# Optimization experiments

Measured on AMD Instinct MI355X. Metric: run time of the kernel, lower is better.

Reference implementation:

```python
import jax, jax.numpy as jnp
import numpy as np

LOW_DIM, SKIP_DIM, OUT_DIM = 512, 256, 256
EPS_IDW = 1e-8
EPS_LN = 1e-5
K = 3


def setup_inputs() -> dict:
    key = jax.random.key(0)
    ks = jax.random.split(key, 10)
    B, N, S = 4, 8192, 2048
    xyz_hi = jax.random.uniform(ks[0], (B, N, 3), dtype=jnp.float32)
    xyz_lo = jax.random.uniform(ks[1], (B, S, 3), dtype=jnp.float32)
    feat_skip = jax.random.normal(ks[2], (B, N, SKIP_DIM), dtype=jnp.float32)
    feat_lo = jax.random.normal(ks[3], (B, S, LOW_DIM), dtype=jnp.float32)
    in_dim = LOW_DIM + SKIP_DIM
    W1 = jax.random.normal(ks[4], (in_dim, OUT_DIM), dtype=jnp.float32) / np.sqrt(in_dim)
    b1 = jnp.zeros((OUT_DIM,), dtype=jnp.float32)
    W2 = jax.random.normal(ks[5], (OUT_DIM, OUT_DIM), dtype=jnp.float32) / np.sqrt(OUT_DIM)
    b2 = jnp.zeros((OUT_DIM,), dtype=jnp.float32)
    gamma = jnp.ones((OUT_DIM,), dtype=jnp.float32)
    beta = jnp.zeros((OUT_DIM,), dtype=jnp.float32)
    return {"xyz_hi": xyz_hi, "xyz_lo": xyz_lo, "feat_skip": feat_skip,
            "feat_lo": feat_lo, "W1": W1, "b1": b1, "W2": W2, "b2": b2,
            "gamma": gamma, "beta": beta}


def _layer_norm(x, gamma, beta):
    mu = jnp.mean(x, axis=-1, keepdims=True)
    var = jnp.mean(jnp.square(x - mu), axis=-1, keepdims=True)
    return (x - mu) * jax.lax.rsqrt(var + EPS_LN) * gamma + beta


def reference(xyz_hi, xyz_lo, feat_skip, feat_lo, W1, b1, W2, b2, gamma, beta):
    B, N, _ = xyz_hi.shape
    _, S, _ = xyz_lo.shape
    if S == 1:
        interpolated = jnp.broadcast_to(feat_lo, (B, N, feat_lo.shape[-1]))
    else:
        # pairwise Euclidean distances: (B, N, S)
        d2 = (jnp.sum(xyz_hi ** 2, -1)[:, :, None]
              + jnp.sum(xyz_lo ** 2, -1)[:, None, :]
              - 2.0 * jnp.einsum('bnd,bsd->bns', xyz_hi, xyz_lo))
        dists = jnp.sqrt(jnp.maximum(d2, 0.0))
        # smallest-3 via top_k on negated distances
        neg_d, knn_idx = jax.lax.top_k(-dists, K)          # (B, N, 3)
        dk = -neg_d
        inv_d = 1.0 / (dk + EPS_IDW)
        weights = inv_d / jnp.sum(inv_d, axis=-1, keepdims=True)  # (B, N, 3)
        # gather neighbor features: (B, N, 3, low_dim)
        knn_feat = feat_lo[jnp.arange(B)[:, None, None], knn_idx]
        interpolated = jnp.einsum('bnk,bnkc->bnc', weights, knn_feat)
    fused = jnp.concatenate([feat_skip, interpolated], axis=-1)   # (B, N, skip+low)
    h = jax.nn.relu(fused @ W1 + b1)
    h = h @ W2 + b2
    return _layer_norm(h, gamma, beta)
```

## Files before the change

kernel.cpp:

```cpp
#include <hip/hip_runtime.h>
#include <hip/hip_bf16.h>
#include <stdint.h>

typedef unsigned short u16;
typedef __attribute__((ext_vector_type(8))) short short8;
typedef __attribute__((ext_vector_type(4))) float f32x4;

#define BB 4
#define NN 8192
#define SS 2048
#define MTOT 32768
#define CSKIP 256
#define CLO 512
#define CIN 768
#define COUT 256

__device__ __forceinline__ u16 f2bf(float f) {
  unsigned u = __float_as_uint(f);
  u += 0x7fffu + ((u >> 16) & 1u);
  return (u16)(u >> 16);
}

__device__ __forceinline__ void gl_lds16(const void* g, void* l) {
  __builtin_amdgcn_global_load_lds(
      (const __attribute__((address_space(1))) void*)g,
      (__attribute__((address_space(3))) void*)l, 16, 0, 0);
}

__global__ __launch_bounds__(256) void wconv_kernel(const float* __restrict__ W1,
                                                    const float* __restrict__ W2,
                                                    u16* __restrict__ W1aT,
                                                    u16* __restrict__ W1bT,
                                                    u16* __restrict__ W2T) {
  int i = blockIdx.x * 256 + threadIdx.x;
  if (i < 65536) {
    int n = i >> 8, k = i & 255;
    W1aT[i] = f2bf(W1[(size_t)k * COUT + n]);
  } else if (i < 65536 + 131072) {
    int j = i - 65536;
    int n = j >> 9, k = j & 511;
    W1bT[j] = f2bf(W1[(size_t)(256 + k) * COUT + n]);
  } else {
    int j = i - 65536 - 131072;
    int n = j >> 8, k = j & 255;
    W2T[j] = f2bf(W2[(size_t)k * COUT + n]);
  }
}

__global__ __launch_bounds__(512) void knn_kernel(
    const float* __restrict__ xyz_hi, const float* __restrict__ xyz_lo,
    float* __restrict__ wq_g, int* __restrict__ iq_g) {
  __shared__ float4 sxyz[SS];
  __shared__ float md[8][64][3];
  __shared__ int   mi[8][64][3];

  int tid = threadIdx.x;
  int blk = blockIdx.x;
  int b = blk >> 7;
  const float* xl = xyz_lo + (size_t)b * SS * 3;
  for (int j = tid; j < SS; j += 512)
    sxyz[j] = make_float4(xl[j * 3 + 0], xl[j * 3 + 1], xl[j * 3 + 2], 0.f);
  __syncthreads();

  int wave = tid >> 6, lane = tid & 63;
  int qm = blk * 64 + lane;
  float qx = xyz_hi[(size_t)qm * 3 + 0];
  float qy = xyz_hi[(size_t)qm * 3 + 1];
  float qz = xyz_hi[(size_t)qm * 3 + 2];

  float b0 = 1e30f, b1 = 1e30f, b2 = 1e30f;
  int i0 = -1, i1 = -1, i2 = -1;
  int j0 = wave * 256;
#pragma unroll 8
  for (int jj = 0; jj < 256; ++jj) {
    int j = j0 + jj;
    float4 p = sxyz[j];
    float dx = p.x - qx, dy = p.y - qy, dz = p.z - qz;
    float d = fmaf(dx, dx, fmaf(dy, dy, dz * dz));
    bool c0 = d < b0, c1 = d < b1, c2 = d < b2;
    float nb0 = fminf(b0, d);
    float nb1 = __builtin_amdgcn_fmed3f(b0, b1, d);
    float nb2 = __builtin_amdgcn_fmed3f(b1, b2, d);
    int ni0 = c0 ? j : i0;
    int ni1 = c0 ? i0 : (c1 ? j : i1);
    int ni2 = c1 ? i1 : (c2 ? j : i2);
    b0 = nb0; b1 = nb1; b2 = nb2;
    i0 = ni0; i1 = ni1; i2 = ni2;
  }
  md[wave][lane][0] = b0; mi[wave][lane][0] = i0;
  md[wave][lane][1] = b1; mi[wave][lane][1] = i1;
  md[wave][lane][2] = b2; mi[wave][lane][2] = i2;
  __syncthreads();

  if (tid < 64) {
    int q = tid;
    float fb0 = 1e30f, fb1 = 1e30f, fb2 = 1e30f;
    int fi0 = -1, fi1 = -1, fi2 = -1;
    for (int p = 0; p < 8; ++p)
#pragma unroll
      for (int s = 0; s < 3; ++s) {
        float d = md[p][q][s]; int ix = mi[p][q][s];
        if (d < fb2 || (d == fb2 && ix < fi2)) {
          fb2 = d; fi2 = ix;
          if (fb2 < fb1 || (fb2 == fb1 && fi2 < fi1)) {
            float t = fb1; fb1 = fb2; fb2 = t; int ti = fi1; fi1 = fi2; fi2 = ti;
          }
          if (fb1 < fb0 || (fb1 == fb0 && fi1 < fi0)) {
            float t = fb0; fb0 = fb1; fb1 = t; int ti = fi0; fi0 = fi1; fi1 = ti;
          }
        }
      }
    int qm2 = blk * 64 + q;
    float d0 = sqrtf(fb0), d1 = sqrtf(fb1), d2 = sqrtf(fb2);
    float inv0 = 1.0f / (d0 + 1e-8f);
    float inv1 = 1.0f / (d1 + 1e-8f);
    float inv2 = 1.0f / (d2 + 1e-8f);
    float s = inv0 + inv1 + inv2;
    wq_g[(size_t)qm2 * 3 + 0] = inv0 / s;
    wq_g[(size_t)qm2 * 3 + 1] = inv1 / s;
    wq_g[(size_t)qm2 * 3 + 2] = inv2 / s;
    iq_g[(size_t)qm2 * 3 + 0] = fi0;
    iq_g[(size_t)qm2 * 3 + 1] = fi1;
    iq_g[(size_t)qm2 * 3 + 2] = fi2;
  }
}

__global__ __launch_bounds__(256, 4) void ggemm_kernel(
    const float* __restrict__ feat_lo, const u16* __restrict__ W1bT,
    float* __restrict__ G) {
  __shared__ u16 As[32 * 40];
  __shared__ u16 Bs[256 * 32];
  int tid = threadIdx.x;
  int m0 = blockIdx.x << 5;
  int w = tid >> 6, lane = tid & 63;
  int quad = lane >> 4, l16 = lane & 15;

  int srow = tid >> 3, s4 = (tid & 7) << 2;
  const float* arow = feat_lo + (size_t)(m0 + srow) * CLO + s4;
  u16* As_dst = As + srow * 40 + s4;

  f32x4 zero = {0.f, 0.f, 0.f, 0.f};
  f32x4 acc[2][4];
#pragma unroll
  for (int tm = 0; tm < 2; ++tm)
#pragma unroll
    for (int tn = 0; tn < 4; ++tn) acc[tm][tn] = zero;

  for (int kc = 0; kc < 16; ++kc) {
    __syncthreads();
#pragma unroll
    for (int r = 0; r < 4; ++r) {
      int u = tid + r * 256;
      int nrow = u >> 2, c = u & 3;
      int cg = c ^ (nrow & 3);
      gl_lds16(W1bT + (size_t)nrow * CLO + kc * 32 + cg * 8, (char*)Bs + u * 16);
    }
    float4 av = *(const float4*)(arow + kc * 32);
    union { __hip_bfloat162 h2[2]; uint2 u2; } pk;
    pk.h2[0] = __float22bfloat162_rn(make_float2(av.x, av.y));
    pk.h2[1] = __float22bfloat162_rn(make_float2(av.z, av.w));
    *(uint2*)As_dst = pk.u2;
    __syncthreads();

    short8 af[2], bf[4];
#pragma unroll
    for (int t = 0; t < 2; ++t)
      af[t] = *(const short8*)(As + (t * 16 + l16) * 40 + quad * 8);
#pragma unroll
    for (int t = 0; t < 4; ++t) {
      int rr = w * 64 + t * 16 + l16;
      bf[t] = *(const short8*)(Bs + (rr * 4 + (quad ^ (rr & 3))) * 8);
    }
#pragma unroll
    for (int tm = 0; tm < 2; ++tm)
#pragma unroll
      for (int tn = 0; tn < 4; ++tn)
        acc[tm][tn] = __builtin_amdgcn_mfma_f32_16x16x32_bf16(af[tm], bf[tn], acc[tm][tn], 0, 0, 0);
  }

#pragma unroll
  for (int tm = 0; tm < 2; ++tm)
#pragma unroll
    for (int tn = 0; tn < 4; ++tn) {
      int col = w * 64 + tn * 16 + l16;
#pragma unroll
      for (int r = 0; r < 4; ++r) {
        int row = m0 + tm * 16 + quad * 4 + r;
        G[(size_t)row * COUT + col] = acc[tm][tn][r];
      }
    }
}

__global__ __launch_bounds__(256, 2) void gemm1p_kernel(
    const float* __restrict__ feat_skip, const u16* __restrict__ W1aT,
    const float* __restrict__ b1, const float* __restrict__ G,
    const float* __restrict__ wq_g, const int* __restrict__ iq_g,
    u16* __restrict__ H) {
  __shared__ u16 As[64 * 40];
  __shared__ u16 Bs[256 * 32];
  __shared__ float swq[192];
  __shared__ int   siq[192];
  int tid = threadIdx.x;
  int m0 = blockIdx.x << 6;
  int bS = (m0 >> 13) * SS;
  int w = tid >> 6, lane = tid & 63;
  int quad = lane >> 4, l16 = lane & 15;

  if (tid < 192) {
    swq[tid] = wq_g[(size_t)m0 * 3 + tid];
    siq[tid] = iq_g[(size_t)m0 * 3 + tid];
  }

  int srow = tid >> 2, sc8 = (tid & 3) << 3;
  const float* arow = feat_skip + (size_t)(m0 + srow) * CSKIP + sc8;
  u16* As_dst = As + srow * 40 + sc8;

  f32x4 zero = {0.f, 0.f, 0.f, 0.f};
  f32x4 acc[4][4];
#pragma unroll
  for (int tm = 0; tm < 4; ++tm)
#pragma unroll
    for (int tn = 0; tn < 4; ++tn) acc[tm][tn] = zero;

  for (int kc = 0; kc < 8; ++kc) {
    __syncthreads();
#pragma unroll
    for (int r = 0; r < 4; ++r) {
      int u = tid + r * 256;
      int nrow = u >> 2, c = u & 3;
      int cg = c ^ (nrow & 3);
      gl_lds16(W1aT + (size_t)nrow * CSKIP + kc * 32 + cg * 8, (char*)Bs + u * 16);
    }
    float4 x0 = *(const float4*)(arow + kc * 32);
    float4 x1 = *(const float4*)(arow + kc * 32 + 4);
    union { __hip_bfloat162 h2[4]; uint4 u4; } pk;
    pk.h2[0] = __float22bfloat162_rn(make_float2(x0.x, x0.y));
    pk.h2[1] = __float22bfloat162_rn(make_float2(x0.z, x0.w));
    pk.h2[2] = __float22bfloat162_rn(make_float2(x1.x, x1.y));
    pk.h2[3] = __float22bfloat162_rn(make_float2(x1.z, x1.w));
    *(uint4*)As_dst = pk.u4;
    __syncthreads();

    short8 af[4], bf[4];
#pragma unroll
    for (int t = 0; t < 4; ++t)
      af[t] = *(const short8*)(As + (t * 16 + l16) * 40 + quad * 8);
#pragma unroll
    for (int t = 0; t < 4; ++t) {
      int rr = w * 64 + t * 16 + l16;
      bf[t] = *(const short8*)(Bs + (rr * 4 + (quad ^ (rr & 3))) * 8);
    }
#pragma unroll
    for (int tm = 0; tm < 4; ++tm)
#pragma unroll
      for (int tn = 0; tn < 4; ++tn)
        acc[tm][tn] = __builtin_amdgcn_mfma_f32_16x16x32_bf16(af[tm], bf[tn], acc[tm][tn], 0, 0, 0);
  }

  float bias[4];
#pragma unroll
  for (int tn = 0; tn < 4; ++tn) bias[tn] = b1[w * 64 + tn * 16 + l16];

#pragma unroll
  for (int tm = 0; tm < 4; ++tm)
#pragma unroll
    for (int r = 0; r < 4; ++r) {
      int rl = tm * 16 + quad * 4 + r;
      float w0 = swq[rl * 3 + 0], w1 = swq[rl * 3 + 1], w2 = swq[rl * 3 + 2];
      const float* g0 = G + (size_t)(bS + siq[rl * 3 + 0]) * COUT;
      const float* g1 = G + (size_t)(bS + siq[rl * 3 + 1]) * COUT;
      const float* g2 = G + (size_t)(bS + siq[rl * 3 + 2]) * COUT;
#pragma unroll
      for (int tn = 0; tn < 4; ++tn) {
        int col = w * 64 + tn * 16 + l16;
        float gv = fmaf(w0, g0[col], fmaf(w1, g1[col], w2 * g2[col]));
        float v = acc[tm][tn][r] + bias[tn] + gv;
        v = v > 0.f ? v : 0.f;
        H[(size_t)(m0 + rl) * COUT + col] = f2bf(v);
      }
    }
}

__global__ __launch_bounds__(256, 2) void gemm2_ln_kernel(const u16* __restrict__ H,
                                                          const u16* __restrict__ Bt,
                                                          const float* __restrict__ b2,
                                                          const float* __restrict__ gamma,
                                                          const float* __restrict__ beta,
                                                          float* __restrict__ out) {
  __shared__ u16 As[64 * 64];
  __shared__ u16 Bs[256 * 64];
  __shared__ float red[4][64][2];
  __shared__ float stats[64][2];
  int tid = threadIdx.x;
  int m0 = blockIdx.x << 6;
  int w = tid >> 6, lane = tid & 63;
  int quad = lane >> 4, l16 = lane & 15;

  f32x4 zero = {0.f, 0.f, 0.f, 0.f};
  f32x4 acc[4][4];
#pragma unroll
  for (int tm = 0; tm < 4; ++tm)
#pragma unroll
    for (int tn = 0; tn < 4; ++tn) acc[tm][tn] = zero;

  for (int kc = 0; kc < 4; ++kc) {
    __syncthreads();
#pragma unroll
    for (int r = 0; r < 2; ++r) {
      int u = tid + r * 256;
      int row = u >> 3, c = u & 7;
      int cg = c ^ (row & 7);
      gl_lds16(H + (size_t)(m0 + row) * COUT + kc * 64 + cg * 8, (char*)As + u * 16);
    }
#pragma unroll
    for (int r = 0; r < 8; ++r) {
      int u = tid + r * 256;
      int nrow = u >> 3, c = u & 7;
      int cg = c ^ (nrow & 7);
      gl_lds16(Bt + (size_t)nrow * COUT + kc * 64 + cg * 8, (char*)Bs + u * 16);
    }
    __syncthreads();

#pragma unroll
    for (int ko = 0; ko < 2; ++ko) {
      int ck = ko * 4 + quad;
      short8 af[4], bf[4];
#pragma unroll
      for (int t = 0; t < 4; ++t) {
        int ra = t * 16 + l16;
        af[t] = *(const short8*)(As + (ra * 8 + (ck ^ (ra & 7))) * 8);
      }
#pragma unroll
      for (int t = 0; t < 4; ++t) {
        int rr = w * 64 + t * 16 + l16;
        bf[t] = *(const short8*)(Bs + (rr * 8 + (ck ^ (rr & 7))) * 8);
      }
#pragma unroll
      for (int tm = 0; tm < 4; ++tm)
#pragma unroll
        for (int tn = 0; tn < 4; ++tn)
          acc[tm][tn] = __builtin_amdgcn_mfma_f32_16x16x32_bf16(af[tm], bf[tn], acc[tm][tn], 0, 0, 0);
    }
  }

  float bias[4], g[4], be[4];
#pragma unroll
  for (int tn = 0; tn < 4; ++tn) {
    int col = w * 64 + tn * 16 + l16;
    bias[tn] = b2[col]; g[tn] = gamma[col]; be[tn] = beta[col];
  }
#pragma unroll
  for (int tm = 0; tm < 4; ++tm)
#pragma unroll
    for (int r = 0; r < 4; ++r) {
      float s = 0.f, sq = 0.f;
#pragma unroll
      for (int tn = 0; tn < 4; ++tn) {
        float v = acc[tm][tn][r] + bias[tn];
        acc[tm][tn][r] = v;
        s += v; sq += v * v;
      }
#pragma unroll
      for (int msk = 1; msk < 16; msk <<= 1) {
        s += __shfl_xor(s, msk);
        sq += __shfl_xor(sq, msk);
      }
      if (l16 == 0) {
        int rl = tm * 16 + quad * 4 + r;
        red[w][rl][0] = s;
        red[w][rl][1] = sq;
      }
    }
  __syncthreads();
  if (tid < 64) {
    float s = red[0][tid][0] + red[1][tid][0] + red[2][tid][0] + red[3][tid][0];
    float sq = red[0][tid][1] + red[1][tid][1] + red[2][tid][1] + red[3][tid][1];
    float mu = s * (1.f / 256.f);
    float var = sq * (1.f / 256.f) - mu * mu;
    stats[tid][0] = mu;
    stats[tid][1] = rsqrtf(var + 1e-5f);
  }
  __syncthreads();
#pragma unroll
  for (int tm = 0; tm < 4; ++tm)
#pragma unroll
    for (int r = 0; r < 4; ++r) {
      int rl = tm * 16 + quad * 4 + r;
      float mu = stats[rl][0], rstd = stats[rl][1];
#pragma unroll
      for (int tn = 0; tn < 4; ++tn) {
        int col = w * 64 + tn * 16 + l16;
        out[(size_t)(m0 + rl) * COUT + col] = (acc[tm][tn][r] - mu) * rstd * g[tn] + be[tn];
      }
    }
}

extern "C" void kernel_launch(void* const* d_in, const int* in_sizes, int n_in,
                              void* d_out, int out_size, void* d_ws, size_t ws_size,
                              hipStream_t stream) {
  const float* xyz_hi    = (const float*)d_in[0];
  const float* xyz_lo    = (const float*)d_in[1];
  const float* feat_skip = (const float*)d_in[2];
  const float* feat_lo   = (const float*)d_in[3];
  const float* W1        = (const float*)d_in[4];
  const float* b1        = (const float*)d_in[5];
  const float* W2        = (const float*)d_in[6];
  const float* b2        = (const float*)d_in[7];
  const float* gamma     = (const float*)d_in[8];
  const float* beta      = (const float*)d_in[9];
  float* out = (float*)d_out;

  char* ws = (char*)d_ws;
  u16*   H     = (u16*)ws;
  u16*   W1aT  = (u16*)(ws + 16777216);
  u16*   W1bT  = (u16*)(ws + 16908288);
  u16*   W2T   = (u16*)(ws + 17170432);
  float* wq_g  = (float*)(ws + 17301504);
  int*   iq_g  = (int*)(ws + 17694720);
  float* G     = (float*)(ws + 18087936);

  wconv_kernel<<<1024, 256, 0, stream>>>(W1, W2, W1aT, W1bT, W2T);
  knn_kernel<<<MTOT / 64, 512, 0, stream>>>(xyz_hi, xyz_lo, wq_g, iq_g);
  ggemm_kernel<<<(BB * SS) / 32, 256, 0, stream>>>(feat_lo, W1bT, G);
  gemm1p_kernel<<<MTOT / 64, 256, 0, stream>>>(feat_skip, W1aT, b1, G, wq_g, iq_g, H);
  gemm2_ln_kernel<<<MTOT / 64, 256, 0, stream>>>(H, W2T, b2, gamma, beta, out);
}
```

Baseline: 187.6 us.

## Fuse GEMM1 and GEMM2+LayerNorm via LDS, merge weight conversion into KNN kernel

The hidden activation H now stays in shared memory (Hs) inside one kernel that runs GEMM1, bias, ReLU and the interpolation, then GEMM2 and LayerNorm. This removes the global write and read of H and one launch. The weight bf16 conversion moves into extra blocks of the KNN kernel, and the KNN top-3 update is guarded by a branch that is skipped when d is not below the current third-best. The fused kernel uses more LDS (about 34KB for Hs), which may lower occupancy, and the branch can cause wave divergence.

```diff
diff --git a/kernel.cpp b/kernel.cpp
--- a/kernel.cpp
+++ b/kernel.cpp
@@ -27,35 +27,36 @@
       (__attribute__((address_space(3))) void*)l, 16, 0, 0);
 }
 
-__global__ __launch_bounds__(256) void wconv_kernel(const float* __restrict__ W1,
-                                                    const float* __restrict__ W2,
-                                                    u16* __restrict__ W1aT,
-                                                    u16* __restrict__ W1bT,
-                                                    u16* __restrict__ W2T) {
-  int i = blockIdx.x * 256 + threadIdx.x;
-  if (i < 65536) {
-    int n = i >> 8, k = i & 255;
-    W1aT[i] = f2bf(W1[(size_t)k * COUT + n]);
-  } else if (i < 65536 + 131072) {
-    int j = i - 65536;
-    int n = j >> 9, k = j & 511;
-    W1bT[j] = f2bf(W1[(size_t)(256 + k) * COUT + n]);
-  } else {
-    int j = i - 65536 - 131072;
-    int n = j >> 8, k = j & 255;
-    W2T[j] = f2bf(W2[(size_t)k * COUT + n]);
-  }
-}
-
-__global__ __launch_bounds__(512) void knn_kernel(
+__global__ __launch_bounds__(512) void knn_wconv_kernel(
     const float* __restrict__ xyz_hi, const float* __restrict__ xyz_lo,
-    float* __restrict__ wq_g, int* __restrict__ iq_g) {
+    const float* __restrict__ W1, const float* __restrict__ W2,
+    float* __restrict__ wq_g, int* __restrict__ iq_g,
+    u16* __restrict__ W1aT, u16* __restrict__ W1bT, u16* __restrict__ W2T) {
+  int blk = blockIdx.x;
+  if (blk >= 512) {
+    int base = (blk - 512) * 512 + threadIdx.x;
+    for (int i = base; i < 262144; i += 65536) {
+      if (i < 65536) {
+        int n = i >> 8, k = i & 255;
+        W1aT[i] = f2bf(W1[(size_t)k * COUT + n]);
+      } else if (i < 196608) {
+        int j = i - 65536;
+        int n = j >> 9, k = j & 511;
+        W1bT[j] = f2bf(W1[(size_t)(256 + k) * COUT + n]);
+      } else {
+        int j = i - 196608;
+        int n = j >> 8, k = j & 255;
+        W2T[j] = f2bf(W2[(size_t)k * COUT + n]);
+      }
+    }
+    return;
+  }
+
   __shared__ float4 sxyz[SS];
   __shared__ float md[8][64][3];
   __shared__ int   mi[8][64][3];
 
   int tid = threadIdx.x;
-  int blk = blockIdx.x;
   int b = blk >> 7;
   const float* xl = xyz_lo + (size_t)b * SS * 3;
   for (int j = tid; j < SS; j += 512)
@@ -71,21 +72,22 @@
   float b0 = 1e30f, b1 = 1e30f, b2 = 1e30f;
   int i0 = -1, i1 = -1, i2 = -1;
   int j0 = wave * 256;
-#pragma unroll 8
+#pragma unroll 4
   for (int jj = 0; jj < 256; ++jj) {
     int j = j0 + jj;
     float4 p = sxyz[j];
     float dx = p.x - qx, dy = p.y - qy, dz = p.z - qz;
     float d = fmaf(dx, dx, fmaf(dy, dy, dz * dz));
-    bool c0 = d < b0, c1 = d < b1, c2 = d < b2;
-    float nb0 = fminf(b0, d);
-    float nb1 = __builtin_amdgcn_fmed3f(b0, b1, d);
-    float nb2 = __builtin_amdgcn_fmed3f(b1, b2, d);
-    int ni0 = c0 ? j : i0;
-    int ni1 = c0 ? i0 : (c1 ? j : i1);
-    int ni2 = c1 ? i1 : (c2 ? j : i2);
-    b0 = nb0; b1 = nb1; b2 = nb2;
-    i0 = ni0; i1 = ni1; i2 = ni2;
+    if (d < b2) {
+      bool c0 = d < b0, c1 = d < b1;
+      float nb0 = fminf(b0, d);
+      float nb1 = __builtin_amdgcn_fmed3f(b0, b1, d);
+      float nb2 = c1 ? b1 : d;
+      i2 = c1 ? i1 : j;
+      i1 = c0 ? i0 : (c1 ? j : i1);
+      i0 = c0 ? j : i0;
+      b0 = nb0; b1 = nb1; b2 = nb2;
+    }
   }
   md[wave][lane][0] = b0; mi[wave][lane][0] = i0;
   md[wave][lane][1] = b1; mi[wave][lane][1] = i1;
@@ -191,15 +193,20 @@
     }
 }
 
-__global__ __launch_bounds__(256, 2) void gemm1p_kernel(
+__global__ __launch_bounds__(256, 2) void gemm12_kernel(
     const float* __restrict__ feat_skip, const u16* __restrict__ W1aT,
     const float* __restrict__ b1, const float* __restrict__ G,
     const float* __restrict__ wq_g, const int* __restrict__ iq_g,
-    u16* __restrict__ H) {
+    const u16* __restrict__ W2T, const float* __restrict__ b2,
+    const float* __restrict__ gamma, const float* __restrict__ beta,
+    float* __restrict__ out) {
+  __shared__ u16 Hs[64 * 264];
+  __shared__ u16 Bs[256 * 32];
   __shared__ u16 As[64 * 40];
-  __shared__ u16 Bs[256 * 32];
   __shared__ float swq[192];
   __shared__ int   siq[192];
+  __shared__ float red[4][64][2];
+  __shared__ float stats[64][2];
   int tid = threadIdx.x;
   int m0 = blockIdx.x << 6;
   int bS = (m0 >> 13) * SS;
@@ -257,90 +264,60 @@
         acc[tm][tn] = __builtin_amdgcn_mfma_f32_16x16x32_bf16(af[tm], bf[tn], acc[tm][tn], 0, 0, 0);
   }
 
-  float bias[4];
-#pragma unroll
-  for (int tn = 0; tn < 4; ++tn) bias[tn] = b1[w * 64 + tn * 16 + l16];
+  {
+    float bias[4];
+#pragma unroll
+    for (int tn = 0; tn < 4; ++tn) bias[tn] = b1[w * 64 + tn * 16 + l16];
+#pragma unroll
+    for (int tm = 0; tm < 4; ++tm)
+#pragma unroll
+      for (int r = 0; r < 4; ++r) {
+        int rl = tm * 16 + quad * 4 + r;
+        float w0 = swq[rl * 3 + 0], w1 = swq[rl * 3 + 1], w2 = swq[rl * 3 + 2];
+        const float* g0 = G + (size_t)(bS + siq[rl * 3 + 0]) * COUT;
+        const float* g1 = G + (size_t)(bS + siq[rl * 3 + 1]) * COUT;
+        const float* g2 = G + (size_t)(bS + siq[rl * 3 + 2]) * COUT;
+#pragma unroll
+        for (int tn = 0; tn < 4; ++tn) {
+          int col = w * 64 + tn * 16 + l16;
+          float gv = fmaf(w0, g0[col], fmaf(w1, g1[col], w2 * g2[col]));
+          float v = acc[tm][tn][r] + bias[tn] + gv;
+          v = v > 0.f ? v : 0.f;
+          Hs[rl * 264 + col] = f2bf(v);
+        }
+      }
+  }
 
 #pragma unroll
   for (int tm = 0; tm < 4; ++tm)
 #pragma unroll
+    for (int tn = 0; tn < 4; ++tn) acc[tm][tn] = zero;
+
+  for (int kc = 0; kc < 8; ++kc) {
+    __syncthreads();
+#pragma unroll
     for (int r = 0; r < 4; ++r) {
-      int rl = tm * 16 + quad * 4 + r;
-      float w0 = swq[rl * 3 + 0], w1 = swq[rl * 3 + 1], w2 = swq[rl * 3 + 2];
-      const float* g0 = G + (size_t)(bS + siq[rl * 3 + 0]) * COUT;
-      const float* g1 = G + (size_t)(bS + siq[rl * 3 + 1]) * COUT;
-      const float* g2 = G + (size_t)(bS + siq[rl * 3 + 2]) * COUT;
-#pragma unroll
-      for (int tn = 0; tn < 4; ++tn) {
-        int col = w * 64 + tn * 16 + l16;
-        float gv = fmaf(w0, g0[col], fmaf(w1, g1[col], w2 * g2[col]));
-        float v = acc[tm][tn][r] + bias[tn] + gv;
-        v = v > 0.f ? v : 0.f;
-        H[(size_t)(m0 + rl) * COUT + col] = f2bf(v);
-      }
-    }
-}
-
-__global__ __launch_bounds__(256, 2) void gemm2_ln_kernel(const u16* __restrict__ H,
-                                                          const u16* __restrict__ Bt,
-                                                          const float* __restrict__ b2,
-                                                          const float* __restrict__ gamma,
-                                                          const float* __restrict__ beta,
-                                                          float* __restrict__ out) {
-  __shared__ u16 As[64 * 64];
-  __shared__ u16 Bs[256 * 64];
-  __shared__ float red[4][64][2];
-  __shared__ float stats[64][2];
-  int tid = threadIdx.x;
-  int m0 = blockIdx.x << 6;
-  int w = tid >> 6, lane = tid & 63;
-  int quad = lane >> 4, l16 = lane & 15;
-
-  f32x4 zero = {0.f, 0.f, 0.f, 0.f};
-  f32x4 acc[4][4];
-#pragma unroll
-  for (int tm = 0; tm < 4; ++tm)
-#pragma unroll
-    for (int tn = 0; tn < 4; ++tn) acc[tm][tn] = zero;
-
-  for (int kc = 0; kc < 4; ++kc) {
-    __syncthreads();
-#pragma unroll
-    for (int r = 0; r < 2; ++r) {
       int u = tid + r * 256;
-      int row = u >> 3, c = u & 7;
-      int cg = c ^ (row & 7);
-      gl_lds16(H + (size_t)(m0 + row) * COUT + kc * 64 + cg * 8, (char*)As + u * 16);
-    }
-#pragma unroll
-    for (int r = 0; r < 8; ++r) {
-      int u = tid + r * 256;
-      int nrow = u >> 3, c = u & 7;
-      int cg = c ^ (nrow & 7);
-      gl_lds16(Bt + (size_t)nrow * COUT + kc * 64 + cg * 8, (char*)Bs + u * 16);
-    }
-    __syncthreads();
-
-#pragma unroll
-    for (int ko = 0; ko < 2; ++ko) {
-      int ck = ko * 4 + quad;
-      short8 af[4], bf[4];
-#pragma unroll
-      for (int t = 0; t < 4; ++t) {
-        int ra = t * 16 + l16;
-        af[t] = *(const short8*)(As + (ra * 8 + (ck ^ (ra & 7))) * 8);
-      }
-#pragma unroll
-      for (int t = 0; t < 4; ++t) {
-        int rr = w * 64 + t * 16 + l16;
-        bf[t] = *(const short8*)(Bs + (rr * 8 + (ck ^ (rr & 7))) * 8);
-      }
-#pragma unroll
-      for (int tm = 0; tm < 4; ++tm)
-#pragma unroll
-        for (int tn = 0; tn < 4; ++tn)
-          acc[tm][tn] = __builtin_amdgcn_mfma_f32_16x16x32_bf16(af[tm], bf[tn], acc[tm][tn], 0, 0, 0);
-    }
+      int nrow = u >> 2, c = u & 3;
+      int cg = c ^ (nrow & 3);
+      gl_lds16(W2T + (size_t)nrow * COUT + kc * 32 + cg * 8, (char*)Bs + u * 16);
+    }
+    __syncthreads();
+
+    short8 af[4], bf[4];
+#pragma unroll
+    for (int t = 0; t < 4; ++t)
+      af[t] = *(const short8*)(Hs + (t * 16 + l16) * 264 + kc * 32 + quad * 8);
+#pragma unroll
+    for (int t = 0; t < 4; ++t) {
+      int rr = w * 64 + t * 16 + l16;
+      bf[t] = *(const short8*)(Bs + (rr * 4 + (quad ^ (rr & 3))) * 8);
+    }
+#pragma unroll
+    for (int tm = 0; tm < 4; ++tm)
+#pragma unroll
+      for (int tn = 0; tn < 4; ++tn)
+        acc[tm][tn] = __builtin_amdgcn_mfma_f32_16x16x32_bf16(af[tm], bf[tn], acc[tm][tn], 0, 0, 0);
   }
 
   float bias[4], g[4], be[4];
@@ -411,7 +388,6 @@
   float* out = (float*)d_out;
 
   char* ws = (char*)d_ws;
-  u16*   H     = (u16*)ws;
   u16*   W1aT  = (u16*)(ws + 16777216);
   u16*   W1bT  = (u16*)(ws + 16908288);
   u16*   W2T   = (u16*)(ws + 17170432);
@@ -419,9 +395,9 @@
   int*   iq_g  = (int*)(ws + 17694720);
   float* G     = (float*)(ws + 18087936);
 
-  wconv_kernel<<<1024, 256, 0, stream>>>(W1, W2, W1aT, W1bT, W2T);
-  knn_kernel<<<MTOT / 64, 512, 0, stream>>>(xyz_hi, xyz_lo, wq_g, iq_g);
+  knn_wconv_kernel<<<640, 512, 0, stream>>>(xyz_hi, xyz_lo, W1, W2,
+                                            wq_g, iq_g, W1aT, W1bT, W2T);
   ggemm_kernel<<<(BB * SS) / 32, 256, 0, stream>>>(feat_lo, W1bT, G);
-  gemm1p_kernel<<<MTOT / 64, 256, 0, stream>>>(feat_skip, W1aT, b1, G, wq_g, iq_g, H);
-  gemm2_ln_kernel<<<MTOT / 64, 256, 0, stream>>>(H, W2T, b2, gamma, beta, out);
-}
+  gemm12_kernel<<<MTOT / 64, 256, 0, stream>>>(feat_skip, W1aT, b1, G, wq_g, iq_g,
+                                               W2T, b2, gamma, beta, out);
+}
```

Result: no change. 185.9 us (-0.9%).
